# Performance work log

Measured on AMD Instinct MI355X. Metric: run time of the kernel, lower is better.

## Reference

```python
import jax, jax.numpy as jnp
import numpy as np

N_HEADS = 16
EPS = -1e9  # masking constant from the original module


def setup_inputs() -> dict:
    key = jax.random.key(0)
    ks = jax.random.split(key, 5)
    B, S, D = 2, 2048, 1024
    x = jax.random.normal(ks[0], (B, S, D), dtype=jnp.float32)
    attention_mask = jax.random.randint(ks[1], (B, S), 0, 2, dtype=jnp.int32)
    W_qkv_kernel = jax.random.normal(ks[2], (D, 3 * D), dtype=jnp.float32) * (D ** -0.5)
    W_qkv_bias = jnp.zeros((3 * D,), dtype=jnp.float32)
    c_proj_kernel = jax.random.normal(ks[3], (D, D), dtype=jnp.float32) * (D ** -0.5)
    c_proj_bias = jnp.zeros((D,), dtype=jnp.float32)
    return {"x": x, "attention_mask": attention_mask,
            "W_qkv_kernel": W_qkv_kernel, "W_qkv_bias": W_qkv_bias,
            "c_proj_kernel": c_proj_kernel, "c_proj_bias": c_proj_bias}


def reference(x, attention_mask, W_qkv_kernel, W_qkv_bias, c_proj_kernel, c_proj_bias):
    B, S, D = x.shape
    H = N_HEADS
    Dh = D // H
    qkv = x @ W_qkv_kernel + W_qkv_bias                  # [B,S,3D]
    q, k, v = jnp.split(qkv, 3, axis=-1)
    # [B,S,D] -> [B,H,S,Dh]
    q = q.reshape(B, S, H, Dh).transpose(0, 2, 1, 3)
    k = k.reshape(B, S, H, Dh).transpose(0, 2, 1, 3)
    v = v.reshape(B, S, H, Dh).transpose(0, 2, 1, 3)
    scores = jnp.einsum('bhqd,bhkd->bhqk', q, k)          # [B,H,S,S]
    # NOTE: original applies masks BEFORE scaling; keep that order faithfully.
    pad = attention_mask[:, None, None, :] == 0           # [B,1,1,S]
    scores = jnp.where(pad, EPS, scores)
    causal = jnp.tril(jnp.ones((S, S), dtype=bool))
    scores = jnp.where(causal[None, None, :, :], scores, EPS)
    scaled = scores / jnp.sqrt(jnp.float32(Dh))
    attn = jax.nn.softmax(scaled, axis=-1)
    ctx = jnp.einsum('bhqk,bhkd->bhqd', attn, v)          # [B,H,S,Dh]
    ctx = ctx.transpose(0, 2, 1, 3).reshape(B, S, D)
    return ctx @ c_proj_kernel + c_proj_bias
```

## Files before the change

kernel.cpp:

```cpp
#include <hip/hip_runtime.h>
#include <hip/hip_bf16.h>
#include <stdint.h>

typedef __bf16 bf16_t;
typedef __bf16 bf16x4_t __attribute__((ext_vector_type(4)));
typedef __bf16 bf16x8_t __attribute__((ext_vector_type(8)));
typedef float f32x4_t __attribute__((ext_vector_type(4)));
typedef unsigned int u32x2_t __attribute__((ext_vector_type(2)));

#define S_LEN   2048
#define DMODEL  1024
#define NH      16
#define DH      64
#define LOG2E   1.4426950408889634f
#define SCL     (0.125f * LOG2E)
#define EPS2    (-1.8033688e8f)

#define MFMA(a, b, c) __builtin_amdgcn_mfma_f32_16x16x32_bf16(a, b, c, 0, 0, 0)

#define GLOAD_LDS16(gsrc, ldst)                                         \
  __builtin_amdgcn_global_load_lds(                                     \
      (__attribute__((address_space(1))) void*)(void*)(gsrc),           \
      (__attribute__((address_space(3))) void*)(void*)(ldst), 16, 0, 0)

__global__ void k_cvt_bf16(const float* __restrict__ in, bf16_t* __restrict__ out,
                           const int* __restrict__ am, float* __restrict__ mskf,
                           int n4, int nmask) {
  int i = blockIdx.x * blockDim.x + threadIdx.x;
  if (i < nmask) mskf[i] = am[i] ? 0.f : EPS2;
  if (i >= n4) return;
  float4 v = reinterpret_cast<const float4*>(in)[i];
  bf16x4_t o = {(bf16_t)v.x, (bf16_t)v.y, (bf16_t)v.z, (bf16_t)v.w};
  reinterpret_cast<bf16x4_t*>(out)[i] = o;
}

__global__ void k_transpose_bf16(const float* __restrict__ in, bf16_t* __restrict__ out,
                                 int R, int C) {
  __shared__ float tile[32][33];
  int c0 = blockIdx.x * 32, r0 = blockIdx.y * 32;
  int tx = threadIdx.x, ty = threadIdx.y;
  for (int i = ty; i < 32; i += 8)
    tile[i][tx] = in[(size_t)(r0 + i) * C + (c0 + tx)];
  __syncthreads();
  for (int i = ty; i < 32; i += 8)
    out[(size_t)(c0 + i) * R + (r0 + tx)] = (bf16_t)tile[tx][i];
}

template<int MODE>
__global__ __launch_bounds__(256, 2)
void k_gemm(const bf16_t* __restrict__ A, const bf16_t* __restrict__ Bt,
            const float* __restrict__ bias,
            bf16_t* __restrict__ Qb, bf16_t* __restrict__ Kb, bf16_t* __restrict__ Vt,
            float* __restrict__ Out, int M, int N, int K) {
  constexpr int BN  = (MODE == 0) ? 192 : 64;
  constexpr int JN  = BN / 32;
  constexpr int BST = BN / 32;
  __shared__ alignas(16) bf16_t As[2][128 * 64];
  __shared__ alignas(16) bf16_t Bs[2][BN * 64];
  const int tid = threadIdx.x;
  const int lane = tid & 63;
  const int w = tid >> 6;
  const int hl = blockIdx.y * gridDim.x + blockIdx.x;
  const int xcd = hl & 7, tt = hl >> 3;
  const int mb = ((xcd >> 1) << 3) + (tt >> 3);
  const int nb = ((xcd & 1) << 3) + (tt & 7);
  const int m0 = mb * 128;
  const int n0 = nb * BN;
  const int wm = (w >> 1) * 64, wn = (w & 1) * (BN / 2);
  const int l15 = lane & 15, lg = lane >> 4;
  const int lrow = lane >> 3;
  const int lcsw = (((lane & 7) ^ lrow) * 8);
  const int swz8 = (l15 & 7) * 8;

  f32x4_t acc[4][JN] = {};

#define GSTAGE(k0_, buf_)                                                        \
  do {                                                                           \
    _Pragma("unroll")                                                            \
    for (int p = 0; p < 4; ++p) {                                                \
      const int rb = w * 32 + p * 8;                                             \
      GLOAD_LDS16(&A[(size_t)(m0 + rb + lrow) * K + (k0_) + lcsw],               \
                  &As[buf_][rb * 64]);                                           \
    }                                                                            \
    _Pragma("unroll")                                                            \
    for (int p = 0; p < BST; ++p) {                                              \
      const int rb = w * (BST * 8) + p * 8;                                      \
      GLOAD_LDS16(&Bt[(size_t)(n0 + rb + lrow) * K + (k0_) + lcsw],              \
                  &Bs[buf_][rb * 64]);                                           \
    }                                                                            \
  } while (0)

  GSTAGE(0, 0);
  int buf = 0;
  for (int k0 = 0; k0 < K; k0 += 64) {
    if (k0 + 64 < K) {
      GSTAGE(k0 + 64, buf ^ 1);
      if (MODE == 0) asm volatile("s_waitcnt vmcnt(10)" ::: "memory");
      else           asm volatile("s_waitcnt vmcnt(6)"  ::: "memory");
    } else {
      asm volatile("s_waitcnt vmcnt(0)" ::: "memory");
    }
    __builtin_amdgcn_s_barrier();
    __builtin_amdgcn_sched_barrier(0);
    const bf16_t* Asb = As[buf];
    const bf16_t* Bsb = Bs[buf];
#pragma unroll
    for (int kk = 0; kk < 64; kk += 32) {
      bf16x8_t a[4], b[JN];
      const int kof = kk + 8 * lg;
#pragma unroll
      for (int i = 0; i < 4; ++i)
        a[i] = *reinterpret_cast<const bf16x8_t*>(
            &Asb[(wm + i * 16 + l15) * 64 + (kof ^ swz8)]);
#pragma unroll
      for (int j = 0; j < JN; ++j)
        b[j] = *reinterpret_cast<const bf16x8_t*>(
            &Bsb[(wn + j * 16 + l15) * 64 + (kof ^ swz8)]);
      __builtin_amdgcn_s_setprio(1);
#pragma unroll
      for (int i = 0; i < 4; ++i)
#pragma unroll
        for (int j = 0; j < JN; ++j)
          acc[i][j] = MFMA(a[i], b[j], acc[i][j]);
      __builtin_amdgcn_s_setprio(0);
    }
    __builtin_amdgcn_sched_barrier(0);
    __builtin_amdgcn_s_barrier();
    buf ^= 1;
  }
#undef GSTAGE

  const int rbase = lg * 4;
#pragma unroll
  for (int i = 0; i < 4; ++i)
#pragma unroll
    for (int j = 0; j < JN; ++j) {
      const int ncol = n0 + wn + j * 16 + l15;
      const float bs = bias[ncol];
      if (MODE == 1) {
#pragma unroll
        for (int r = 0; r < 4; ++r) {
          int m = m0 + wm + i * 16 + rbase + r;
          Out[(size_t)m * N + ncol] = acc[i][j][r] + bs;
        }
      } else {
        const int mrow0 = m0 + wm + i * 16 + rbase;
        const int b2 = mrow0 >> 11, s0 = mrow0 & 2047;
        const int t = ncol >> 10, nn = ncol & 1023;
        const int h = nn >> 6, d = nn & 63;
        const size_t bh = (size_t)b2 * NH + h;
        if (t == 2) {
          bf16x4_t o;
#pragma unroll
          for (int r = 0; r < 4; ++r) o[r] = (bf16_t)(acc[i][j][r] + bs);
          *reinterpret_cast<bf16x4_t*>(&Vt[(bh * DH + d) * S_LEN + s0]) = o;
        } else {
          bf16_t* dst = (t == 0 ? Qb : Kb) + (bh * S_LEN + s0) * DH + d;
#pragma unroll
          for (int r = 0; r < 4; ++r)
            dst[(size_t)r * DH] = (bf16_t)(acc[i][j][r] + bs);
        }
      }
    }
}

__global__ __launch_bounds__(256)
void k_vmean(const bf16_t* __restrict__ Vt, float* __restrict__ vmean) {
  const int bh = blockIdx.x;
  const int t = threadIdx.x;
  const int d = t >> 2, q = t & 3;
  const bf16_t* vp = Vt + ((size_t)bh * DH + d) * S_LEN + q * 512;
  float s = 0.f;
  for (int i = 0; i < 512; i += 8) {
    bf16x8_t v = *reinterpret_cast<const bf16x8_t*>(&vp[i]);
    for (int j = 0; j < 8; ++j) s += (float)v[j];
  }
  __shared__ float part[256];
  part[t] = s;
  __syncthreads();
  if (q == 0)
    vmean[bh * DH + d] = (part[t] + part[t + 1] + part[t + 2] + part[t + 3]) * (1.f / 2048.f);
}

__global__ __launch_bounds__(512, 2)
void k_attn(const bf16_t* __restrict__ Qb, const bf16_t* __restrict__ Kb,
            const bf16_t* __restrict__ Vt, const float* __restrict__ mskf,
            const float* __restrict__ vmean, bf16_t* __restrict__ ctxb) {
  extern __shared__ char smem[];
  const int tid = threadIdx.x, lane = tid & 63, w = tid >> 6;
  const int wg = w >> 2, wl = w & 3;
  const int bh = blockIdx.x, b = bh >> 4, hh = bh & 15;
  const int pr = blockIdx.y;
  const int l15 = lane & 15, lg = lane >> 4;
  const bf16_t* Qp = Qb + (size_t)bh * S_LEN * DH;
  const char*   Kg = (const char*)(Kb + (size_t)bh * S_LEN * DH);
  const char*   Vg = (const char*)(Vt + (size_t)bh * DH * S_LEN);
  const float*  mp = mskf + b * S_LEN;

  const int srow = lane >> 3;
  const int scol = ((lane & 7) * 16) ^ (srow * 16);
  const int vrow = lane >> 4;
  const int swz  = 16 * (l15 & 7);
  char* gbase = smem + wg * 65536;

#define STAGE_PH(ph_, buf_)                                                        \
  do {                                                                             \
    const int kb_ = (ph_) * 128;                                                   \
    _Pragma("unroll")                                                              \
    for (int jj = 0; jj < 4; ++jj) {                                               \
      const int rk = wl * 32 + jj * 8;                                             \
      GLOAD_LDS16(Kg + (size_t)(kb_ + rk + srow) * 128 + scol,                     \
                  gbase + (buf_) * 16384 + rk * 128);                              \
      const int rv = wl * 16 + jj * 4;                                             \
      const int vc = ((lane & 15) * 16) ^ ((((jj << 2) + vrow) & 7) * 16);         \
      GLOAD_LDS16(Vg + (size_t)(rv + vrow) * 4096 + (size_t)kb_ * 2 + vc,          \
                  gbase + 32768 + (buf_) * 16384 + rv * 256);                      \
    }                                                                              \
  } while (0)

#define QK_SUB(S_, STA, STB)                                                       \
  _Pragma("unroll")                                                                \
  for (int t = 0; t < 4; ++t) {                                                    \
    const int rbyte = ((S_) * 64 + t * 16 + l15) * 128;                            \
    bf16x8_t k0 = *reinterpret_cast<const bf16x8_t*>(Ksb + rbyte + ((16 * lg) ^ swz));       \
    bf16x8_t k1 = *reinterpret_cast<const bf16x8_t*>(Ksb + rbyte + ((64 + 16 * lg) ^ swz));  \
    f32x4_t s = {}; s = MFMA(k0, qA0, s); s = MFMA(k1, qA1, s); STA[t] = s;        \
    f32x4_t s2 = {}; s2 = MFMA(k0, qB0, s2); s2 = MFMA(k1, qB1, s2); STB[t] = s2;  \
  }

#define SM_PACK(ST, MK, LACC, PF, QG, CAUSAL, KB0)                                 \
  do {                                                                             \
    float e[16];                                                                   \
    float ps0 = 0.f, ps1 = 0.f, ps2 = 0.f, ps3 = 0.f;                              \
    _Pragma("unroll")                                                              \
    for (int t = 0; t < 4; ++t)                                                    \
      _Pragma("unroll")                                                            \
      for (int r = 0; r < 4; ++r) {                                                \
        float v = fmaf(ST[t][r], SCL, MK[t][r]);                                   \
        if (CAUSAL) {                                                              \
          int k = (KB0) + t * 16 + lg * 4 + r;                                     \
          v = (k <= (QG)) ? v : EPS2;                                              \
        }                                                                          \
        float ex = __builtin_amdgcn_exp2f(v);                                      \
        e[t * 4 + r] = ex;                                                         \
        if (t == 0) ps0 += ex; else if (t == 1) ps1 += ex;                         \
        else if (t == 2) ps2 += ex; else ps3 += ex;                                \
      }                                                                            \
    LACC += (ps0 + ps1) + (ps2 + ps3);                                             \
    _Pragma("unroll")                                                              \
    for (int g = 0; g < 2; ++g) {                                                  \
      union { uint32_t u2[4]; bf16x8_t v; } pk_;                                   \
      _Pragma("unroll")                                                            \
      for (int jj = 0; jj < 4; ++jj)                                               \
        asm("v_cvt_pk_bf16_f32 %0, %1, %2"                                         \
            : "=v"(pk_.u2[jj]) : "v"(e[8 * g + 2 * jj]), "v"(e[8 * g + 2 * jj + 1])); \
      PF[g] = pk_.v;                                                               \
    }                                                                              \
  } while (0)

#define PV_SUB(S_, PFA, PFB)                                                       \
  _Pragma("unroll")                                                                \
  for (int g = 0; g < 2; ++g)                                                      \
    _Pragma("unroll")                                                              \
    for (int f = 0; f < 4; ++f) {                                                  \
      const int rbyte = (f * 16 + l15) * 256;                                      \
      const int cb = (S_) * 128 + 64 * g + 8 * lg;                                 \
      u32x2_t va = *reinterpret_cast<const u32x2_t*>(Vsb + rbyte + (cb ^ swz));         \
      u32x2_t vb = *reinterpret_cast<const u32x2_t*>(Vsb + rbyte + ((cb + 32) ^ swz));  \
      union { uint32_t u2[4]; bf16x8_t v; } vv_;                                   \
      vv_.u2[0] = va[0]; vv_.u2[1] = va[1]; vv_.u2[2] = vb[0]; vv_.u2[3] = vb[1];  \
      poA[f] = MFMA(vv_.v, PFA[g], poA[f]);                                        \
      poB[f] = MFMA(vv_.v, PFB[g], poB[f]);                                        \
    }

  auto run_stripe = [&](int s) {
    const int qbase = s * 128 + wl * 32;
    const int qg0 = qbase + l15, qg1 = qbase + 16 + l15;
    const bf16x8_t qA0 = *reinterpret_cast<const bf16x8_t*>(&Qp[qg0 * DH + 8 * lg]);
    const bf16x8_t qA1 = *reinterpret_cast<const bf16x8_t*>(&Qp[qg0 * DH + 32 + 8 * lg]);
    const bf16x8_t qB0 = *reinterpret_cast<const bf16x8_t*>(&Qp[qg1 * DH + 8 * lg]);
    const bf16x8_t qB1 = *reinterpret_cast<const bf16x8_t*>(&Qp[qg1 * DH + 32 + 8 * lg]);
    f32x4_t poA[4] = {}, poB[4] = {};
    float lA = 0.f, lB = 0.f;
    const int hs = (s + 2) >> 1;

    __syncthreads();
    int buf = 0;
    if (wg == 0) STAGE_PH(0, 0);
    else if (hs <= s) STAGE_PH(hs, 0);

    for (int i = 0; i < hs; ++i) {
      __syncthreads();
      if (wg == 0) { if (i + 1 < hs) STAGE_PH(i + 1, buf ^ 1); }
      else         { if (hs + i + 1 <= s) STAGE_PH(hs + i + 1, buf ^ 1); }
      const int p = (wg == 0) ? i : hs + i;
      if (wg == 0 || p <= s) {
        const char* Ksb = gbase + buf * 16384;
        const char* Vsb = gbase + 32768 + buf * 16384;
        const int kb = p * 128;
        f32x4_t mk0[4], mk1[4];
#pragma unroll
        for (int t = 0; t < 4; ++t) {
          mk0[t] = *reinterpret_cast<const f32x4_t*>(&mp[kb + t * 16 + lg * 4]);
          mk1[t] = *reinterpret_cast<const f32x4_t*>(&mp[kb + 64 + t * 16 + lg * 4]);
        }
        f32x4_t stA0[4], stB0[4], stA1[4], stB1[4];
        bf16x8_t pfA[2], pfB[2];
        if (p < s) {
          __builtin_amdgcn_s_setprio(1);
          QK_SUB(0, stA0, stB0);
          QK_SUB(1, stA1, stB1);
          __builtin_amdgcn_s_setprio(0);
          SM_PACK(stA0, mk0, lA, pfA, qg0, false, 0);
          SM_PACK(stB0, mk0, lB, pfB, qg1, false, 0);
          __builtin_amdgcn_s_setprio(1);
          PV_SUB(0, pfA, pfB);
          __builtin_amdgcn_s_setprio(0);
          SM_PACK(stA1, mk1, lA, pfA, qg0, false, 0);
          SM_PACK(stB1, mk1, lB, pfB, qg1, false, 0);
          __builtin_amdgcn_s_setprio(1);
          PV_SUB(1, pfA, pfB);
          __builtin_amdgcn_s_setprio(0);
        } else {
          QK_SUB(0, stA0, stB0);
          SM_PACK(stA0, mk0, lA, pfA, qg0, true, kb);
          SM_PACK(stB0, mk0, lB, pfB, qg1, true, kb);
          PV_SUB(0, pfA, pfB);
          if (wl >= 2) {
            QK_SUB(1, stA1, stB1);
            SM_PACK(stA1, mk1, lA, pfA, qg0, true, kb + 64);
            SM_PACK(stB1, mk1, lB, pfB, qg1, true, kb + 64);
            PV_SUB(1, pfA, pfB);
          }
        }
      }
      buf ^= 1;
    }

    __syncthreads();
    float* mb_ = (float*)(smem + 65536) + ((size_t)wl * 64 + lane) * 36;
    if (wg == 1) {
#pragma unroll
      for (int f = 0; f < 4; ++f) {
        *reinterpret_cast<f32x4_t*>(mb_ + f * 4)      = poA[f];
        *reinterpret_cast<f32x4_t*>(mb_ + 16 + f * 4) = poB[f];
      }
      mb_[32] = lA; mb_[33] = lB;
    }
    __syncthreads();
    if (wg == 0) {
#pragma unroll
      for (int f = 0; f < 4; ++f) {
        poA[f] += *reinterpret_cast<const f32x4_t*>(mb_ + f * 4);
        poB[f] += *reinterpret_cast<const f32x4_t*>(mb_ + 16 + f * 4);
      }
      lA += mb_[32]; lB += mb_[33];
      lA += __shfl_xor(lA, 16); lA += __shfl_xor(lA, 32);
      lB += __shfl_xor(lB, 16); lB += __shfl_xor(lB, 32);
      const float* vm = vmean + bh * DH;
      {
        const bool dead = (lA == 0.f);
        const float inv = dead ? 0.f : 1.0f / lA;
        bf16_t* orow = ctxb + (size_t)(b * S_LEN + qg0) * DMODEL + hh * DH;
#pragma unroll
        for (int f = 0; f < 4; ++f) {
          bf16x4_t o;
#pragma unroll
          for (int r = 0; r < 4; ++r) {
            int d = f * 16 + lg * 4 + r;
            o[r] = (bf16_t)(dead ? vm[d] : poA[f][r] * inv);
          }
          *reinterpret_cast<bf16x4_t*>(&orow[f * 16 + lg * 4]) = o;
        }
      }
      {
        const bool dead = (lB == 0.f);
        const float inv = dead ? 0.f : 1.0f / lB;
        bf16_t* orow = ctxb + (size_t)(b * S_LEN + qg1) * DMODEL + hh * DH;
#pragma unroll
        for (int f = 0; f < 4; ++f) {
          bf16x4_t o;
#pragma unroll
          for (int r = 0; r < 4; ++r) {
            int d = f * 16 + lg * 4 + r;
            o[r] = (bf16_t)(dead ? vm[d] : poB[f][r] * inv);
          }
          *reinterpret_cast<bf16x4_t*>(&orow[f * 16 + lg * 4]) = o;
        }
      }
    }
  };

  run_stripe(15 - pr);
  run_stripe(pr);
#undef STAGE_PH
#undef QK_SUB
#undef SM_PACK
#undef PV_SUB
}

extern "C" void kernel_launch(void* const* d_in, const int* in_sizes, int n_in,
                              void* d_out, int out_size, void* d_ws, size_t ws_size,
                              hipStream_t stream) {
  const float* x     = (const float*)d_in[0];
  const int*   amask = (const int*)d_in[1];
  const float* Wqkv  = (const float*)d_in[2];
  const float* bqkv  = (const float*)d_in[3];
  const float* Wproj = (const float*)d_in[4];
  const float* bproj = (const float*)d_in[5];
  float* out = (float*)d_out;

  char* ws = (char*)d_ws;
  bf16_t* xb    = (bf16_t*)(ws);
  bf16_t* WqT   = (bf16_t*)(ws + (8llu  << 20));
  bf16_t* WpT   = (bf16_t*)(ws + (14llu << 20));
  bf16_t* Qb    = (bf16_t*)(ws + (16llu << 20));
  bf16_t* Kb    = (bf16_t*)(ws + (24llu << 20));
  bf16_t* Vt    = (bf16_t*)(ws + (32llu << 20));
  bf16_t* ctxb  = (bf16_t*)(ws + (40llu << 20));
  float*  vmean = (float*) (ws + (48llu << 20));
  float*  mskf  = (float*) (ws + (48llu << 20) + 65536);

  k_cvt_bf16<<<4096, 256, 0, stream>>>(x, xb, amask, mskf,
                                       (2 * S_LEN * DMODEL) / 4, 2 * S_LEN);
  k_transpose_bf16<<<dim3(3072 / 32, 1024 / 32), dim3(32, 8), 0, stream>>>(Wqkv, WqT, 1024, 3072);
  k_transpose_bf16<<<dim3(1024 / 32, 1024 / 32), dim3(32, 8), 0, stream>>>(Wproj, WpT, 1024, 1024);
  k_gemm<0><<<dim3(3072 / 192, 4096 / 128), 256, 0, stream>>>(
      xb, WqT, bqkv, Qb, Kb, Vt, nullptr, 4096, 3072, 1024);
  k_vmean<<<32, 256, 0, stream>>>(Vt, vmean);
  k_attn<<<dim3(32, 8), 512, 131072, stream>>>(Qb, Kb, Vt, mskf, vmean, ctxb);
  k_gemm<1><<<dim3(1024 / 64, 4096 / 128), 256, 0, stream>>>(
      ctxb, WpT, bproj, nullptr, nullptr, nullptr, out, 4096, 1024, 1024);
}
```

Measured before the change: 111.5 us.

## Enlarge QKV GEMM tile to 256x192 with 8 waves; merge weight transposes

The QKV projection GEMM now uses 256-row tiles computed by 8 waves per block with dynamic shared memory. The grid is halved to 16x16 and the XCD-aware block mapping is adjusted to match. The two weight-transpose launches are merged into one kernel that picks its matrix by block index. The intent is to reuse each B tile across more rows and save a launch, at the cost of more LDS per block (which may lower occupancy) and a retuned vmcnt wait.

```diff
diff --git a/kernel.cpp b/kernel.cpp
--- a/kernel.cpp
+++ b/kernel.cpp
@@ -34,10 +34,15 @@
   reinterpret_cast<bf16x4_t*>(out)[i] = o;
 }
 
-__global__ void k_transpose_bf16(const float* __restrict__ in, bf16_t* __restrict__ out,
-                                 int R, int C) {
+__global__ void k_transpose2(const float* __restrict__ Wq, bf16_t* __restrict__ WqT,
+                             const float* __restrict__ Wp, bf16_t* __restrict__ WpT) {
   __shared__ float tile[32][33];
-  int c0 = blockIdx.x * 32, r0 = blockIdx.y * 32;
+  int bx = blockIdx.x;
+  const float* in; bf16_t* out; int C;
+  if (bx < 96) { in = Wq; out = WqT; C = 3072; }
+  else         { in = Wp; out = WpT; C = 1024; bx -= 96; }
+  const int R = 1024;
+  int c0 = bx * 32, r0 = blockIdx.y * 32;
   int tx = threadIdx.x, ty = threadIdx.y;
   for (int i = ty; i < 32; i += 8)
     tile[i][tx] = in[(size_t)(r0 + i) * C + (c0 + tx)];
@@ -47,24 +52,29 @@
 }
 
 template<int MODE>
-__global__ __launch_bounds__(256, 2)
+__global__ __launch_bounds__((MODE == 0) ? 512 : 256, 2)
 void k_gemm(const bf16_t* __restrict__ A, const bf16_t* __restrict__ Bt,
             const float* __restrict__ bias,
             bf16_t* __restrict__ Qb, bf16_t* __restrict__ Kb, bf16_t* __restrict__ Vt,
             float* __restrict__ Out, int M, int N, int K) {
-  constexpr int BN  = (MODE == 0) ? 192 : 64;
-  constexpr int JN  = BN / 32;
-  constexpr int BST = BN / 32;
-  __shared__ alignas(16) bf16_t As[2][128 * 64];
-  __shared__ alignas(16) bf16_t Bs[2][BN * 64];
+  constexpr int BM    = (MODE == 0) ? 256 : 128;
+  constexpr int BN    = (MODE == 0) ? 192 : 64;
+  constexpr int WAVES = (MODE == 0) ? 8 : 4;
+  constexpr int JN    = BN / 32;
+  constexpr int BROWS = BN / WAVES;
+  constexpr int BST   = BROWS / 8;
+  extern __shared__ char gsm[];
+  bf16_t* As0 = (bf16_t*)gsm;
+  bf16_t* Bs0 = (bf16_t*)(gsm + (size_t)2 * BM * 64 * 2);
   const int tid = threadIdx.x;
   const int lane = tid & 63;
   const int w = tid >> 6;
   const int hl = blockIdx.y * gridDim.x + blockIdx.x;
   const int xcd = hl & 7, tt = hl >> 3;
-  const int mb = ((xcd >> 1) << 3) + (tt >> 3);
-  const int nb = ((xcd & 1) << 3) + (tt & 7);
-  const int m0 = mb * 128;
+  int mb, nb;
+  if (MODE == 0) { mb = (xcd >> 1) * 4 + (tt >> 3);   nb = (xcd & 1) * 8 + (tt & 7); }
+  else           { mb = ((xcd >> 1) << 3) + (tt >> 3); nb = ((xcd & 1) << 3) + (tt & 7); }
+  const int m0 = mb * BM;
   const int n0 = nb * BN;
   const int wm = (w >> 1) * 64, wn = (w & 1) * (BN / 2);
   const int l15 = lane & 15, lg = lane >> 4;
@@ -80,13 +90,13 @@
     for (int p = 0; p < 4; ++p) {                                                \
       const int rb = w * 32 + p * 8;                                             \
       GLOAD_LDS16(&A[(size_t)(m0 + rb + lrow) * K + (k0_) + lcsw],               \
-                  &As[buf_][rb * 64]);                                           \
+                  As0 + (size_t)(buf_) * (BM * 64) + rb * 64);                   \
     }                                                                            \
     _Pragma("unroll")                                                            \
     for (int p = 0; p < BST; ++p) {                                              \
-      const int rb = w * (BST * 8) + p * 8;                                      \
+      const int rb = w * BROWS + p * 8;                                          \
       GLOAD_LDS16(&Bt[(size_t)(n0 + rb + lrow) * K + (k0_) + lcsw],              \
-                  &Bs[buf_][rb * 64]);                                           \
+                  Bs0 + (size_t)(buf_) * (BN * 64) + rb * 64);                   \
     }                                                                            \
   } while (0)
 
@@ -95,15 +105,15 @@
   for (int k0 = 0; k0 < K; k0 += 64) {
     if (k0 + 64 < K) {
       GSTAGE(k0 + 64, buf ^ 1);
-      if (MODE == 0) asm volatile("s_waitcnt vmcnt(10)" ::: "memory");
-      else           asm volatile("s_waitcnt vmcnt(6)"  ::: "memory");
+      if (MODE == 0) asm volatile("s_waitcnt vmcnt(7)" ::: "memory");
+      else           asm volatile("s_waitcnt vmcnt(6)" ::: "memory");
     } else {
       asm volatile("s_waitcnt vmcnt(0)" ::: "memory");
     }
     __builtin_amdgcn_s_barrier();
     __builtin_amdgcn_sched_barrier(0);
-    const bf16_t* Asb = As[buf];
-    const bf16_t* Bsb = Bs[buf];
+    const bf16_t* Asb = As0 + (size_t)buf * (BM * 64);
+    const bf16_t* Bsb = Bs0 + (size_t)buf * (BN * 64);
 #pragma unroll
     for (int kk = 0; kk < 64; kk += 32) {
       bf16x8_t a[4], b[JN];
@@ -423,12 +433,11 @@
 
   k_cvt_bf16<<<4096, 256, 0, stream>>>(x, xb, amask, mskf,
                                        (2 * S_LEN * DMODEL) / 4, 2 * S_LEN);
-  k_transpose_bf16<<<dim3(3072 / 32, 1024 / 32), dim3(32, 8), 0, stream>>>(Wqkv, WqT, 1024, 3072);
-  k_transpose_bf16<<<dim3(1024 / 32, 1024 / 32), dim3(32, 8), 0, stream>>>(Wproj, WpT, 1024, 1024);
-  k_gemm<0><<<dim3(3072 / 192, 4096 / 128), 256, 0, stream>>>(
+  k_transpose2<<<dim3(128, 32), dim3(32, 8), 0, stream>>>(Wqkv, WqT, Wproj, WpT);
+  k_gemm<0><<<dim3(16, 16), 512, 114688, stream>>>(
       xb, WqT, bqkv, Qb, Kb, Vt, nullptr, 4096, 3072, 1024);
   k_vmean<<<32, 256, 0, stream>>>(Vt, vmean);
   k_attn<<<dim3(32, 8), 512, 131072, stream>>>(Qb, Kb, Vt, mskf, vmean, ctxb);
-  k_gemm<1><<<dim3(1024 / 64, 4096 / 128), 256, 0, stream>>>(
+  k_gemm<1><<<dim3(16, 32), 256, 49152, stream>>>(
       ctxb, WpT, bproj, nullptr, nullptr, nullptr, out, 4096, 1024, 1024);
 }
```

Measured after the change: 108.6 us. 1.03x faster.
